# Performance work log

Measured on AMD Instinct MI355X. Metric: run time of the kernel, lower is better.

Reference implementation:

```python
import jax, jax.numpy as jnp
import numpy as np

OUT_FEATURES = 4096
IN_FEATURES = 4096

# NF4 codebook (bitsandbytes normal-float 4-bit values)
_NF4_CODEBOOK = np.array([
    -1.0, -0.6961928, -0.52507305, -0.3949175, -0.28444138, -0.18477343,
    -0.09105004, 0.0, 0.0795803, 0.1609302, 0.2461123, 0.33791524,
    0.44070983, 0.562617, 0.72295684, 1.0], dtype=np.float32)


def setup_inputs() -> dict:
    key = jax.random.key(0)
    k_x, k_codes, k_scale, k_bias = jax.random.split(key, 4)
    x = jax.random.normal(k_x, (4, 2048, IN_FEATURES), dtype=jnp.float32)
    # packed uint8 nibble codes stored as int32 in [0, 256)
    packed_codes = jax.random.randint(
        k_codes, (OUT_FEATURES * IN_FEATURES // 2,), 0, 256, dtype=jnp.int32)
    # positive per-channel scales [out, 1]
    scale = jax.random.uniform(k_scale, (OUT_FEATURES, 1), dtype=jnp.float32) * 0.05 + 0.01
    bias = jax.random.normal(k_bias, (OUT_FEATURES,), dtype=jnp.float32)
    return {"x": x, "packed_codes": packed_codes, "scale": scale, "bias": bias}


def _dequantize_nf4(packed_codes, scale):
    codebook = jnp.asarray(_NF4_CODEBOOK)
    low = packed_codes & 15           # even positions
    high = (packed_codes >> 4) & 15   # odd positions
    # interleave: unpacked[0::2]=low, unpacked[1::2]=high
    idx = jnp.stack([low, high], axis=-1).reshape(-1)  # [out*in]
    w = codebook[idx].reshape(OUT_FEATURES, IN_FEATURES) * scale  # [out, in]
    return w


def reference(x, packed_codes, scale, bias):
    w = _dequantize_nf4(packed_codes, scale)
    # F.linear: x @ w.T + bias
    return jnp.einsum("bsi,oi->bso", x, w) + bias
```

## Files before the change

kernel.cpp:

```cpp
#include <hip/hip_runtime.h>
#include <stdint.h>

#define IN_F 4096
#define OUT_F 4096
#define M_ROWS 8192

__device__ __constant__ int c_nf4_i8[16] = {
    -127, -88, -67, -50, -36, -23, -12, 0, 10, 20, 31, 43, 56, 71, 92, 127};

typedef int i32x4 __attribute__((ext_vector_type(4)));
typedef int i32x16 __attribute__((ext_vector_type(16)));

__global__ __launch_bounds__(256) void k_quant_x(
    const float* __restrict__ x, signed char* __restrict__ xq,
    float* __restrict__ steps) {
  const int row = blockIdx.x;
  const int tid = threadIdx.x;
  const float4* xr = (const float4*)(x + (size_t)row * IN_F);
  float4 v[4];
  float m = 0.0f;
#pragma unroll
  for (int i = 0; i < 4; ++i) {
    v[i] = xr[tid + 256 * i];
    m = fmaxf(m, fmaxf(fmaxf(fabsf(v[i].x), fabsf(v[i].y)),
                       fmaxf(fabsf(v[i].z), fabsf(v[i].w))));
  }
#pragma unroll
  for (int off = 32; off > 0; off >>= 1) m = fmaxf(m, __shfl_xor(m, off));
  __shared__ float wmax[4];
  if ((tid & 63) == 0) wmax[tid >> 6] = m;
  __syncthreads();
  m = fmaxf(fmaxf(wmax[0], wmax[1]), fmaxf(wmax[2], wmax[3]));
  const float inv = (m > 0.0f) ? 127.0f / m : 0.0f;
  if (tid == 0) steps[row] = m * (1.0f / 127.0f);
  int* oq = (int*)(xq + (size_t)row * IN_F);
#pragma unroll
  for (int i = 0; i < 4; ++i) {
    int q0 = (int)rintf(v[i].x * inv);
    int q1 = (int)rintf(v[i].y * inv);
    int q2 = (int)rintf(v[i].z * inv);
    int q3 = (int)rintf(v[i].w * inv);
    oq[tid + 256 * i] =
        (q0 & 255) | ((q1 & 255) << 8) | ((q2 & 255) << 16) | (q3 << 24);
  }
}

__global__ __launch_bounds__(256) void k_dequant(
    const int* __restrict__ packed, signed char* __restrict__ W) {
  __shared__ short lut[256];
  {
    const int b = threadIdx.x;
    const int lo = c_nf4_i8[b & 15], hi = c_nf4_i8[b >> 4];
    lut[b] = (short)((lo & 0xFF) | ((hi & 0xFF) << 8));
  }
  __syncthreads();
  const int tid = blockIdx.x * 256 + threadIdx.x;
  const int4 ca = ((const int4*)packed)[2 * tid];
  const int4 cb = ((const int4*)packed)[2 * tid + 1];
  union { short h[8]; int4 v; } o;
  o.h[0] = lut[ca.x]; o.h[1] = lut[ca.y]; o.h[2] = lut[ca.z]; o.h[3] = lut[ca.w];
  o.h[4] = lut[cb.x]; o.h[5] = lut[cb.y]; o.h[6] = lut[cb.z]; o.h[7] = lut[cb.w];
  ((int4*)W)[tid] = o.v;
}

#define GLL(gptr, lptr)                                          \
  __builtin_amdgcn_global_load_lds(                              \
      (__attribute__((address_space(1))) void*)(gptr),           \
      (__attribute__((address_space(3))) void*)(lptr), 16, 0, 0)

#define FENCE() asm volatile("" ::: "memory")

__device__ __forceinline__ void gemm_phase(
    const signed char* SA, const signed char* SB, int mh, int nh,
    int wm, int wn, int r31, int khalf, int ln7, int w,
    i32x16& acc0, i32x16& acc1,
    const signed char* gsrc, signed char* ldst, int kt, int doStage,
    int waitMode) {
  i32x4 a0[4], a1[4], b[4];
#pragma unroll
  for (int ks = 0; ks < 4; ++ks) {
    const int ch = ((2 * ks + khalf) ^ ln7) * 16;
    a0[ks] = *(const i32x4*)&SA[(wm * 64 + mh * 128 + r31) * 128 + ch];
    a1[ks] = *(const i32x4*)&SA[(wm * 64 + mh * 128 + 32 + r31) * 128 + ch];
    b[ks]  = *(const i32x4*)&SB[(wn * 32 + nh * 128 + r31) * 128 + ch];
  }
  if (doStage) {
#pragma unroll
    for (int g = 0; g < 2; ++g)
      GLL(gsrc + (size_t)(g * 64) * IN_F + (size_t)kt * 128,
          ldst + (g * 64 + w * 8) * 128);
  }
  FENCE();
  __builtin_amdgcn_s_barrier();
  FENCE();
  __builtin_amdgcn_s_setprio(1);
#pragma unroll
  for (int ks = 0; ks < 4; ++ks) {
    acc0 = __builtin_amdgcn_mfma_i32_32x32x32_i8(a0[ks], b[ks], acc0, 0, 0, 0);
    acc1 = __builtin_amdgcn_mfma_i32_32x32x32_i8(a1[ks], b[ks], acc1, 0, 0, 0);
  }
  __builtin_amdgcn_s_setprio(0);
  if (waitMode == 1) {
    asm volatile("s_waitcnt vmcnt(4)" ::: "memory");
  } else if (waitMode == 2) {
    asm volatile("s_waitcnt vmcnt(0)" ::: "memory");
  }
  FENCE();
  __builtin_amdgcn_s_barrier();
  FENCE();
}

__global__ __launch_bounds__(512, 2) void k_gemm(
    const signed char* __restrict__ A,
    const signed char* __restrict__ B,
    const float* __restrict__ steps,
    const float* __restrict__ scale,
    const float* __restrict__ bias,
    float* __restrict__ C) {
  __shared__ __align__(16) signed char sA[2][256 * 128];
  __shared__ __align__(16) signed char sB[2][256 * 128];
  const int tid = threadIdx.x;
  const int lane = tid & 63;
  const int w = tid >> 6;
  const int wm = w >> 2;
  const int wn = w & 3;
  const int r31 = lane & 31;
  const int khalf = lane >> 5;
  const int ln7 = lane & 7;

  const int orig = blockIdx.x;
  const int swz = (orig & 7) * 64 + (orig >> 3);
  const int bn = (swz & 15) * 256;
  const int bm = (swz >> 4) * 256;

  const int tr = w * 8 + (lane >> 3);
  const int schnk = (lane & 7) ^ (lane >> 3);
  const signed char* gA = A + (size_t)(bm + tr) * IN_F + schnk * 16;
  const signed char* gB = B + (size_t)(bn + tr) * IN_F + schnk * 16;

  i32x16 acc[2][2][2] = {};

  auto stage2 = [&](const signed char* gsrc, signed char* ldst, int kt) {
#pragma unroll
    for (int g = 0; g < 2; ++g)
      GLL(gsrc + (size_t)(g * 64) * IN_F + (size_t)kt * 128,
          ldst + (g * 64 + w * 8) * 128);
  };

  stage2(gA, &sA[0][0], 0);
  stage2(gA + (size_t)128 * IN_F, &sA[0][128 * 128], 0);
  stage2(gB, &sB[0][0], 0);
  stage2(gB + (size_t)128 * IN_F, &sB[0][128 * 128], 0);
  stage2(gA, &sA[1][0], 1);
  stage2(gB, &sB[1][0], 1);
  asm volatile("s_waitcnt vmcnt(4)" ::: "memory");
  FENCE();
  __builtin_amdgcn_s_barrier();
  FENCE();

#pragma unroll 1
  for (int it = 0; it < 16; ++it) {
    const int nl = (it < 15) ? 1 : 0;
    const int kY = 2 * it + 1;
    const int kXn = 2 * it + 2;
    const int kYn = 2 * it + 3;
    gemm_phase(sA[0], sB[0], 0, 0, wm, wn, r31, khalf, ln7, w,
               acc[0][0][0], acc[0][1][0],
               gA + (size_t)128 * IN_F, &sA[1][128 * 128], kY, 1, 0);
    gemm_phase(sA[0], sB[0], 0, 1, wm, wn, r31, khalf, ln7, w,
               acc[0][0][1], acc[0][1][1],
               gB + (size_t)128 * IN_F, &sB[1][128 * 128], kY, 1, 0);
    gemm_phase(sA[0], sB[0], 1, 0, wm, wn, r31, khalf, ln7, w,
               acc[1][0][0], acc[1][1][0],
               gA, &sA[0][0], kXn, nl, 0);
    gemm_phase(sA[0], sB[0], 1, 1, wm, wn, r31, khalf, ln7, w,
               acc[1][0][1], acc[1][1][1],
               gB, &sB[0][0], kXn, nl, nl ? 1 : 2);
    gemm_phase(sA[1], sB[1], 0, 0, wm, wn, r31, khalf, ln7, w,
               acc[0][0][0], acc[0][1][0],
               gA + (size_t)128 * IN_F, &sA[0][128 * 128], kXn, nl, 0);
    gemm_phase(sA[1], sB[1], 0, 1, wm, wn, r31, khalf, ln7, w,
               acc[0][0][1], acc[0][1][1],
               gB + (size_t)128 * IN_F, &sB[0][128 * 128], kXn, nl, 0);
    gemm_phase(sA[1], sB[1], 1, 0, wm, wn, r31, khalf, ln7, w,
               acc[1][0][0], acc[1][1][0],
               gA, &sA[1][0], kYn, nl, 0);
    gemm_phase(sA[1], sB[1], 1, 1, wm, wn, r31, khalf, ln7, w,
               acc[1][0][1], acc[1][1][1],
               gB, &sB[1][0], kYn, nl, nl ? 1 : 0);
  }

#pragma unroll
  for (int mh = 0; mh < 2; ++mh) {
#pragma unroll
    for (int f = 0; f < 2; ++f) {
      const int row0 = bm + wm * 64 + mh * 128 + f * 32 + 4 * khalf;
#pragma unroll
      for (int nh = 0; nh < 2; ++nh) {
        const int col = bn + wn * 32 + nh * 128 + r31;
        const float fc = scale[col] * (1.0f / 127.0f);
        const float bv = bias[col];
#pragma unroll
        for (int reg = 0; reg < 16; ++reg) {
          const int row = row0 + (reg & 3) + 8 * (reg >> 2);
          C[(size_t)row * OUT_F + col] =
              (float)acc[mh][f][nh][reg] * (steps[row] * fc) + bv;
        }
      }
    }
  }
}

extern "C" void kernel_launch(void* const* d_in, const int* in_sizes, int n_in,
                              void* d_out, int out_size, void* d_ws, size_t ws_size,
                              hipStream_t stream) {
  const float* x      = (const float*)d_in[0];
  const int* packed   = (const int*)d_in[1];
  const float* scale  = (const float*)d_in[2];
  const float* bias   = (const float*)d_in[3];
  float* out = (float*)d_out;

  signed char* Xq = (signed char*)d_ws;
  signed char* Wq = Xq + (size_t)M_ROWS * IN_F;
  float* steps = (float*)(Wq + (size_t)OUT_F * IN_F);

  k_quant_x<<<M_ROWS, 256, 0, stream>>>(x, Xq, steps);
  k_dequant<<<(OUT_F * IN_F / 2) / (256 * 8), 256, 0, stream>>>(packed, Wq);
  k_gemm<<<(OUT_F / 256) * (M_ROWS / 256), 512, 0, stream>>>(
      Xq, Wq, steps, scale, bias, out);
}
```

Before: 423.4 us.

## Restructure GEMM warp tiling to 128x64 per wave and split phases by k-step

```diff
diff --git a/kernel.cpp b/kernel.cpp
--- a/kernel.cpp
+++ b/kernel.cpp
@@ -71,40 +71,37 @@
 #define FENCE() asm volatile("" ::: "memory")
 
 __device__ __forceinline__ void gemm_phase(
-    const signed char* SA, const signed char* SB, int mh, int nh,
-    int wm, int wn, int r31, int khalf, int ln7, int w,
-    i32x16& acc0, i32x16& acc1,
-    const signed char* gsrc, signed char* ldst, int kt, int doStage,
-    int waitMode) {
-  i32x4 a0[4], a1[4], b[4];
-#pragma unroll
-  for (int ks = 0; ks < 4; ++ks) {
-    const int ch = ((2 * ks + khalf) ^ ln7) * 16;
-    a0[ks] = *(const i32x4*)&SA[(wm * 64 + mh * 128 + r31) * 128 + ch];
-    a1[ks] = *(const i32x4*)&SA[(wm * 64 + mh * 128 + 32 + r31) * 128 + ch];
-    b[ks]  = *(const i32x4*)&SB[(wn * 32 + nh * 128 + r31) * 128 + ch];
-  }
+    const signed char* SA, const signed char* SB, const int ks,
+    const int wm, const int wn, const int r31, const int khalf,
+    const int ln7, const int w, i32x16 (&acc)[4][2],
+    const signed char* gsrc, signed char* ldst, const int kt,
+    const int doStage, const int waitZero) {
+  i32x4 af[4], bf[2];
+  const int ch = ((2 * ks + khalf) ^ ln7) * 16;
+#pragma unroll
+  for (int f = 0; f < 4; ++f)
+    af[f] = *(const i32x4*)&SA[(wm * 128 + f * 32 + r31) * 128 + ch];
+#pragma unroll
+  for (int g = 0; g < 2; ++g)
+    bf[g] = *(const i32x4*)&SB[(wn * 64 + g * 32 + r31) * 128 + ch];
   if (doStage) {
 #pragma unroll
+    for (int st = 0; st < 4; ++st)
+      GLL(gsrc + (size_t)(st * 64) * IN_F + (size_t)kt * 128,
+          ldst + (st * 64 + w * 8) * 128);
+  }
+  FENCE();
+  __builtin_amdgcn_s_barrier();
+  FENCE();
+  __builtin_amdgcn_s_setprio(1);
+#pragma unroll
+  for (int f = 0; f < 4; ++f)
+#pragma unroll
     for (int g = 0; g < 2; ++g)
-      GLL(gsrc + (size_t)(g * 64) * IN_F + (size_t)kt * 128,
-          ldst + (g * 64 + w * 8) * 128);
-  }
-  FENCE();
-  __builtin_amdgcn_s_barrier();
-  FENCE();
-  __builtin_amdgcn_s_setprio(1);
-#pragma unroll
-  for (int ks = 0; ks < 4; ++ks) {
-    acc0 = __builtin_amdgcn_mfma_i32_32x32x32_i8(a0[ks], b[ks], acc0, 0, 0, 0);
-    acc1 = __builtin_amdgcn_mfma_i32_32x32x32_i8(a1[ks], b[ks], acc1, 0, 0, 0);
-  }
+      acc[f][g] =
+          __builtin_amdgcn_mfma_i32_32x32x32_i8(af[f], bf[g], acc[f][g], 0, 0, 0);
   __builtin_amdgcn_s_setprio(0);
-  if (waitMode == 1) {
-    asm volatile("s_waitcnt vmcnt(4)" ::: "memory");
-  } else if (waitMode == 2) {
-    asm volatile("s_waitcnt vmcnt(0)" ::: "memory");
-  }
+  if (waitZero) asm volatile("s_waitcnt vmcnt(0)" ::: "memory");
   FENCE();
   __builtin_amdgcn_s_barrier();
   FENCE();
@@ -138,74 +135,61 @@
   const signed char* gA = A + (size_t)(bm + tr) * IN_F + schnk * 16;
   const signed char* gB = B + (size_t)(bn + tr) * IN_F + schnk * 16;
 
-  i32x16 acc[2][2][2] = {};
-
-  auto stage2 = [&](const signed char* gsrc, signed char* ldst, int kt) {
-#pragma unroll
-    for (int g = 0; g < 2; ++g)
-      GLL(gsrc + (size_t)(g * 64) * IN_F + (size_t)kt * 128,
-          ldst + (g * 64 + w * 8) * 128);
+  i32x16 acc[4][2] = {};
+
+  auto stage4 = [&](const signed char* gsrc, signed char* ldst, int kt) {
+#pragma unroll
+    for (int st = 0; st < 4; ++st)
+      GLL(gsrc + (size_t)(st * 64) * IN_F + (size_t)kt * 128,
+          ldst + (st * 64 + w * 8) * 128);
   };
 
-  stage2(gA, &sA[0][0], 0);
-  stage2(gA + (size_t)128 * IN_F, &sA[0][128 * 128], 0);
-  stage2(gB, &sB[0][0], 0);
-  stage2(gB + (size_t)128 * IN_F, &sB[0][128 * 128], 0);
-  stage2(gA, &sA[1][0], 1);
-  stage2(gB, &sB[1][0], 1);
-  asm volatile("s_waitcnt vmcnt(4)" ::: "memory");
+  stage4(gA, &sA[0][0], 0);
+  stage4(gB, &sB[0][0], 0);
+  stage4(gA, &sA[1][0], 1);
+  stage4(gB, &sB[1][0], 1);
+  asm volatile("s_waitcnt vmcnt(8)" ::: "memory");
   FENCE();
   __builtin_amdgcn_s_barrier();
   FENCE();
 
 #pragma unroll 1
   for (int it = 0; it < 16; ++it) {
-    const int nl = (it < 15) ? 1 : 0;
+    const int stY = (it > 0);
+    const int stX = (it < 15);
     const int kY = 2 * it + 1;
-    const int kXn = 2 * it + 2;
-    const int kYn = 2 * it + 3;
-    gemm_phase(sA[0], sB[0], 0, 0, wm, wn, r31, khalf, ln7, w,
-               acc[0][0][0], acc[0][1][0],
-               gA + (size_t)128 * IN_F, &sA[1][128 * 128], kY, 1, 0);
-    gemm_phase(sA[0], sB[0], 0, 1, wm, wn, r31, khalf, ln7, w,
-               acc[0][0][1], acc[0][1][1],
-               gB + (size_t)128 * IN_F, &sB[1][128 * 128], kY, 1, 0);
-    gemm_phase(sA[0], sB[0], 1, 0, wm, wn, r31, khalf, ln7, w,
-               acc[1][0][0], acc[1][1][0],
-               gA, &sA[0][0], kXn, nl, 0);
-    gemm_phase(sA[0], sB[0], 1, 1, wm, wn, r31, khalf, ln7, w,
-               acc[1][0][1], acc[1][1][1],
-               gB, &sB[0][0], kXn, nl, nl ? 1 : 2);
-    gemm_phase(sA[1], sB[1], 0, 0, wm, wn, r31, khalf, ln7, w,
-               acc[0][0][0], acc[0][1][0],
-               gA + (size_t)128 * IN_F, &sA[0][128 * 128], kXn, nl, 0);
-    gemm_phase(sA[1], sB[1], 0, 1, wm, wn, r31, khalf, ln7, w,
-               acc[0][0][1], acc[0][1][1],
-               gB + (size_t)128 * IN_F, &sB[0][128 * 128], kXn, nl, 0);
-    gemm_phase(sA[1], sB[1], 1, 0, wm, wn, r31, khalf, ln7, w,
-               acc[1][0][0], acc[1][1][0],
-               gA, &sA[1][0], kYn, nl, 0);
-    gemm_phase(sA[1], sB[1], 1, 1, wm, wn, r31, khalf, ln7, w,
-               acc[1][0][1], acc[1][1][1],
-               gB, &sB[1][0], kYn, nl, nl ? 1 : 0);
-  }
-
-#pragma unroll
-  for (int mh = 0; mh < 2; ++mh) {
-#pragma unroll
-    for (int f = 0; f < 2; ++f) {
-      const int row0 = bm + wm * 64 + mh * 128 + f * 32 + 4 * khalf;
-#pragma unroll
-      for (int nh = 0; nh < 2; ++nh) {
-        const int col = bn + wn * 32 + nh * 128 + r31;
-        const float fc = scale[col] * (1.0f / 127.0f);
-        const float bv = bias[col];
-#pragma unroll
-        for (int reg = 0; reg < 16; ++reg) {
-          const int row = row0 + (reg & 3) + 8 * (reg >> 2);
-          C[(size_t)row * OUT_F + col] =
-              (float)acc[mh][f][nh][reg] * (steps[row] * fc) + bv;
-        }
+    const int kX = 2 * it + 2;
+    gemm_phase(sA[0], sB[0], 0, wm, wn, r31, khalf, ln7, w, acc,
+               gA, &sA[1][0], kY, stY, 0);
+    gemm_phase(sA[0], sB[0], 1, wm, wn, r31, khalf, ln7, w, acc,
+               gB, &sB[1][0], kY, stY, 0);
+    gemm_phase(sA[0], sB[0], 2, wm, wn, r31, khalf, ln7, w, acc,
+               gA, &sA[0][0], 0, 0, 0);
+    gemm_phase(sA[0], sB[0], 3, wm, wn, r31, khalf, ln7, w, acc,
+               gA, &sA[0][0], 0, 0, 1);
+    gemm_phase(sA[1], sB[1], 0, wm, wn, r31, khalf, ln7, w, acc,
+               gA, &sA[0][0], kX, stX, 0);
+    gemm_phase(sA[1], sB[1], 1, wm, wn, r31, khalf, ln7, w, acc,
+               gB, &sB[0][0], kX, stX, 0);
+    gemm_phase(sA[1], sB[1], 2, wm, wn, r31, khalf, ln7, w, acc,
+               gA, &sA[0][0], 0, 0, 0);
+    gemm_phase(sA[1], sB[1], 3, wm, wn, r31, khalf, ln7, w, acc,
+               gA, &sA[0][0], 0, 0, 1);
+  }
+
+#pragma unroll
+  for (int f = 0; f < 4; ++f) {
+    const int row0 = bm + wm * 128 + f * 32 + 4 * khalf;
+#pragma unroll
+    for (int g = 0; g < 2; ++g) {
+      const int col = bn + wn * 64 + g * 32 + r31;
+      const float fc = scale[col] * (1.0f / 127.0f);
+      const float bv = bias[col];
+#pragma unroll
+      for (int reg = 0; reg < 16; ++reg) {
+        const int row = row0 + (reg & 3) + 8 * (reg >> 2);
+        C[(size_t)row * OUT_F + col] =
+            (float)acc[f][g][reg] * (steps[row] * fc) + bv;
       }
     }
   }
```

New measurement: 378.7 us. 1.12x faster.
